# Kernel optimization log

Hardware: AMD Instinct MI355X
Metric: run time of the kernel (lower is better)

Reference implementation:

```python
import jax, jax.numpy as jnp
import numpy as np

B, S, D, H = 2, 2048, 1024, 16
HD = D // H

def setup_inputs() -> dict:
    key = jax.random.key(0)
    ks = jax.random.split(key, 9)
    s = 1.0 / np.sqrt(D)
    return {
        "x": jax.random.normal(ks[0], (B, S, D), jnp.float32),
        "Wq": jax.random.normal(ks[1], (D, D), jnp.float32) * s,
        "bq": jnp.zeros((D,), jnp.float32),
        "Wk": jax.random.normal(ks[2], (D, D), jnp.float32) * s,
        "bk": jnp.zeros((D,), jnp.float32),
        "Wv": jax.random.normal(ks[3], (D, D), jnp.float32) * s,
        "bv": jnp.zeros((D,), jnp.float32),
        "Wo": jax.random.normal(ks[4], (D, D), jnp.float32) * s,
        "bo": jnp.zeros((D,), jnp.float32),
    }

def reference(x, Wq, bq, Wk, bk, Wv, bv, Wo, bo):
    b, s, d = x.shape
    def split_heads(t):
        return t.reshape(b, s, H, HD).transpose(0, 2, 1, 3)  # [B,H,S,HD]
    q = split_heads(x @ Wq + bq)
    k = split_heads(x @ Wk + bk)
    v = split_heads(x @ Wv + bv)
    scores = jnp.einsum('bhqd,bhkd->bhqk', q, k) / jnp.sqrt(jnp.float32(HD))
    causal = jnp.tril(jnp.ones((s, s), bool))  # True = keep
    scores = jnp.where(causal, scores, -jnp.inf)
    attn = jax.nn.softmax(scores, axis=-1)
    out = jnp.einsum('bhqk,bhkd->bhqd', attn, v)  # [B,H,S,HD]
    out = out.transpose(0, 2, 1, 3).reshape(b, s, d)
    return out @ Wo + bo
```

## Files before the change

### kernel.cpp

```cpp
#include <hip/hip_runtime.h>

typedef unsigned short u16;
typedef unsigned int u32;
typedef __attribute__((ext_vector_type(8))) short bf16x8;
typedef __attribute__((ext_vector_type(4))) float f32x4;

#define BB 2
#define SS 2048
#define DD 1024
#define HH 16
#define HD 64
#define MM (BB * SS)

__device__ inline float u2f(u32 u) { return __uint_as_float(u); }
__device__ inline u16 f2bf(float f) {
  u32 u = __float_as_uint(f);
  return (u16)((u + 0x7fffu + ((u >> 16) & 1u)) >> 16);
}

__device__ inline int sw(int r, int ci) { return r * 64 + (((ci ^ (r & 7)) & 7) << 3); }

__global__ __launch_bounds__(256) void prep(const float* __restrict__ x, u16* __restrict__ xb,
                                            const float* __restrict__ W0, const float* __restrict__ W1,
                                            const float* __restrict__ W2, const float* __restrict__ W3,
                                            u16* __restrict__ Wt) {
  int z = blockIdx.z;
  int t = threadIdx.x;
  if (z >= 4) {
    int gid = (z - 4) * 256 + blockIdx.y * 16 + blockIdx.x;
    int i = (gid * 256 + t) * 8;
    float4 a = *(const float4*)(x + i);
    float4 b = *(const float4*)(x + i + 4);
    uint4 o;
    o.x = (u32)f2bf(a.x) | ((u32)f2bf(a.y) << 16);
    o.y = (u32)f2bf(a.z) | ((u32)f2bf(a.w) << 16);
    o.z = (u32)f2bf(b.x) | ((u32)f2bf(b.y) << 16);
    o.w = (u32)f2bf(b.z) | ((u32)f2bf(b.w) << 16);
    *(uint4*)(xb + i) = o;
    return;
  }
  const float* W = (z == 0) ? W0 : (z == 1) ? W1 : (z == 2) ? W2 : W3;
  u16* out = Wt + (size_t)z * (DD * DD);
  __shared__ __align__(16) u16 T[64][72];
  int n0 = blockIdx.x * 64, k0 = blockIdx.y * 64;
#pragma unroll
  for (int p = 0; p < 4; ++p) {
    int kr = (t >> 4) + p * 16;
    int c4 = (t & 15) * 4;
    float4 v = *(const float4*)&W[(size_t)(k0 + kr) * DD + n0 + c4];
    T[c4 + 0][kr] = f2bf(v.x);
    T[c4 + 1][kr] = f2bf(v.y);
    T[c4 + 2][kr] = f2bf(v.z);
    T[c4 + 3][kr] = f2bf(v.w);
  }
  __syncthreads();
#pragma unroll
  for (int p = 0; p < 2; ++p) {
    int n = (t >> 3) + p * 32;
    int c8 = (t & 7) * 8;
    uint4 v = *(const uint4*)&T[n][c8];
    *(uint4*)&out[(size_t)(n0 + n) * DD + k0 + c8] = v;
  }
}

__global__ __launch_bounds__(256, 3) void gemm_qkv(const u16* __restrict__ xb, const u16* __restrict__ Wt,
                                                   const float* __restrict__ bq, const float* __restrict__ bk,
                                                   const float* __restrict__ bv,
                                                   u16* __restrict__ Qb, u16* __restrict__ Kb, u16* __restrict__ Vtb) {
  __shared__ __align__(16) u16 As[2][128 * 32];
  __shared__ __align__(16) u16 Bs[2][128 * 32];
  const int tid = threadIdx.x, lane = tid & 63, wv = tid >> 6;
  const int wm = (wv >> 1) * 64, wn = (wv & 1) * 64;
  const int l16 = lane & 15, quad = lane >> 4;

  const int id = blockIdx.x;
  const int xcd = id & 7, inner = id >> 3;
  const int mg = xcd >> 1, ng = xcd & 1;
  const int im = inner & 7, rest = inner >> 3;
  const int in_ = rest & 3, z = rest >> 2;
  const int m0 = (mg * 8 + im) * 128, n0 = (ng * 4 + in_) * 128;

  const u16* Bt = Wt + (size_t)z * (DD * DD);
  const float* bias = (z == 0) ? bq : (z == 1) ? bk : bv;

  const int r0 = tid >> 2, k8 = (tid & 3) << 3;
  const u16* Ap0 = &xb[(size_t)(m0 + r0) * DD + k8];
  const u16* Ap1 = Ap0 + (size_t)64 * DD;
  const u16* Bp0 = &Bt[(size_t)(n0 + r0) * DD + k8];
  const u16* Bp1 = Bp0 + (size_t)64 * DD;

  uint4 a0 = *(const uint4*)Ap0, a1 = *(const uint4*)Ap1;
  uint4 b0 = *(const uint4*)Bp0, b1 = *(const uint4*)Bp1;
  *(uint4*)&As[0][r0 * 32 + k8] = a0;
  *(uint4*)&As[0][(r0 + 64) * 32 + k8] = a1;
  *(uint4*)&Bs[0][r0 * 32 + k8] = b0;
  *(uint4*)&Bs[0][(r0 + 64) * 32 + k8] = b1;
  a0 = *(const uint4*)(Ap0 + 32);
  a1 = *(const uint4*)(Ap1 + 32);
  b0 = *(const uint4*)(Bp0 + 32);
  b1 = *(const uint4*)(Bp1 + 32);
  __syncthreads();

  f32x4 acc[4][4];
  f32x4 zero = {0.f, 0.f, 0.f, 0.f};
#pragma unroll
  for (int i = 0; i < 4; ++i)
#pragma unroll
    for (int j = 0; j < 4; ++j) acc[i][j] = zero;

  for (int kk = 0; kk < 32; ++kk) {
    const int cur = (kk & 1) * 4096;
    bf16x8 af[4], bg[4];
#pragma unroll
    for (int i = 0; i < 4; ++i) {
      af[i] = *(const bf16x8*)&As[0][cur + (wm + i * 16 + l16) * 32 + quad * 8];
      bg[i] = *(const bf16x8*)&Bs[0][cur + (wn + i * 16 + l16) * 32 + quad * 8];
    }
#pragma unroll
    for (int i = 0; i < 4; ++i)
#pragma unroll
      for (int j = 0; j < 4; ++j)
        acc[i][j] = __builtin_amdgcn_mfma_f32_16x16x32_bf16(af[i], bg[j], acc[i][j], 0, 0, 0);
    if (kk + 1 < 32) {
      const int nxt = 4096 - cur;
      *(uint4*)&As[0][nxt + r0 * 32 + k8] = a0;
      *(uint4*)&As[0][nxt + (r0 + 64) * 32 + k8] = a1;
      *(uint4*)&Bs[0][nxt + r0 * 32 + k8] = b0;
      *(uint4*)&Bs[0][nxt + (r0 + 64) * 32 + k8] = b1;
      if (kk + 2 < 32) {
        int ko = (kk + 2) * 32;
        a0 = *(const uint4*)(Ap0 + ko);
        a1 = *(const uint4*)(Ap1 + ko);
        b0 = *(const uint4*)(Bp0 + ko);
        b1 = *(const uint4*)(Bp1 + ko);
      }
    }
    __syncthreads();
  }

  const float qsc = (z == 0) ? 0.180336880f : 1.0f;
  if (z == 2) {
#pragma unroll
    for (int i = 0; i < 4; ++i) {
#pragma unroll
      for (int j = 0; j < 4; ++j) {
        int col = n0 + wn + j * 16 + l16;
        float bcol = bias[col];
        int hh = col >> 6, dd = col & 63;
        int row0 = m0 + wm + i * 16 + quad * 4;
        int bb = row0 >> 11, s0 = row0 & (SS - 1);
        u32 w0 = (u32)f2bf(acc[i][j][0] + bcol) | ((u32)f2bf(acc[i][j][1] + bcol) << 16);
        u32 w1 = (u32)f2bf(acc[i][j][2] + bcol) | ((u32)f2bf(acc[i][j][3] + bcol) << 16);
        uint2 pk; pk.x = w0; pk.y = w1;
        *(uint2*)&Vtb[(((size_t)((bb * HH + hh) * HD + dd)) << 11) + s0] = pk;
      }
    }
  } else {
    u16* out = (z == 0) ? Qb : Kb;
#pragma unroll
    for (int i = 0; i < 4; ++i) {
#pragma unroll
      for (int j = 0; j < 4; ++j) {
        int col = n0 + wn + j * 16 + l16;
        float bcol = bias[col];
        int hh = col >> 6, dd = col & 63;
#pragma unroll
        for (int r = 0; r < 4; ++r) {
          int row = m0 + wm + i * 16 + quad * 4 + r;
          int bb = row >> 11, s = row & (SS - 1);
          out[((size_t)((bb * HH + hh) * SS + s) << 6) | dd] = f2bf((acc[i][j][r] + bcol) * qsc);
        }
      }
    }
  }
}

__global__ __launch_bounds__(256, 3) void gemm_out(const u16* __restrict__ Ub, const u16* __restrict__ Wot,
                                                   const float* __restrict__ bo, float* __restrict__ out) {
  __shared__ __align__(16) u16 As[2][128 * 32];
  __shared__ __align__(16) u16 Bs[2][64 * 32];
  const int tid = threadIdx.x, lane = tid & 63, wv = tid >> 6;
  const int wm = (wv >> 1) * 64, wn = (wv & 1) * 32;
  const int l16 = lane & 15, quad = lane >> 4;
  const int r0 = tid >> 2, k8 = (tid & 3) << 3;

  const int id = blockIdx.x;
  const int xcd = id & 7, inner = id >> 3;
  const int mg = xcd >> 1, ng = xcd & 1;
  const int im = inner & 7, in_ = inner >> 3;
  const int m0 = (mg * 8 + im) * 128, n0 = (ng * 8 + in_) * 64;

  const u16* Ap0 = &Ub[(size_t)(m0 + r0) * DD + k8];
  const u16* Ap1 = Ap0 + (size_t)64 * DD;
  const u16* Bp0 = &Wot[(size_t)(n0 + r0) * DD + k8];

  uint4 a0 = *(const uint4*)Ap0, a1 = *(const uint4*)Ap1, b0 = *(const uint4*)Bp0;
  *(uint4*)&As[0][r0 * 32 + k8] = a0;
  *(uint4*)&As[0][(r0 + 64) * 32 + k8] = a1;
  *(uint4*)&Bs[0][r0 * 32 + k8] = b0;
  a0 = *(const uint4*)(Ap0 + 32);
  a1 = *(const uint4*)(Ap1 + 32);
  b0 = *(const uint4*)(Bp0 + 32);
  __syncthreads();

  f32x4 acc[4][2];
  f32x4 zero = {0.f, 0.f, 0.f, 0.f};
#pragma unroll
  for (int i = 0; i < 4; ++i) { acc[i][0] = zero; acc[i][1] = zero; }

  for (int kk = 0; kk < 32; ++kk) {
    const int curA = (kk & 1) * 4096, curB = (kk & 1) * 2048;
    bf16x8 af[4], bg[2];
#pragma unroll
    for (int i = 0; i < 4; ++i) af[i] = *(const bf16x8*)&As[0][curA + (wm + i * 16 + l16) * 32 + quad * 8];
#pragma unroll
    for (int j = 0; j < 2; ++j) bg[j] = *(const bf16x8*)&Bs[0][curB + (wn + j * 16 + l16) * 32 + quad * 8];
#pragma unroll
    for (int i = 0; i < 4; ++i)
#pragma unroll
      for (int j = 0; j < 2; ++j)
        acc[i][j] = __builtin_amdgcn_mfma_f32_16x16x32_bf16(af[i], bg[j], acc[i][j], 0, 0, 0);
    if (kk + 1 < 32) {
      const int nxtA = 4096 - curA, nxtB = 2048 - curB;
      *(uint4*)&As[0][nxtA + r0 * 32 + k8] = a0;
      *(uint4*)&As[0][nxtA + (r0 + 64) * 32 + k8] = a1;
      *(uint4*)&Bs[0][nxtB + r0 * 32 + k8] = b0;
      if (kk + 2 < 32) {
        int ko = (kk + 2) * 32;
        a0 = *(const uint4*)(Ap0 + ko);
        a1 = *(const uint4*)(Ap1 + ko);
        b0 = *(const uint4*)(Bp0 + ko);
      }
    }
    __syncthreads();
  }

#pragma unroll
  for (int i = 0; i < 4; ++i) {
#pragma unroll
    for (int j = 0; j < 2; ++j) {
      int col = n0 + wn + j * 16 + l16;
      float bcol = bo[col];
#pragma unroll
      for (int r = 0; r < 4; ++r) {
        int row = m0 + wm + i * 16 + quad * 4 + r;
        out[(size_t)row * DD + col] = acc[i][j][r] + bcol;
      }
    }
  }
}

__global__ __launch_bounds__(256, 3) void attention_mfma(const u16* __restrict__ Q, const u16* __restrict__ K,
                                                         const u16* __restrict__ Vt, u16* __restrict__ Uo) {
  const int tid = threadIdx.x, lane = tid & 63, wv = tid >> 6;
  const int l16 = lane & 15, quad = lane >> 4;
  const int bh = blockIdx.x & 31;
  const int b = bh >> 4, h = bh & 15;
  const int qA = blockIdx.x >> 5;
  const int qB = 31 - qA;
  const int q0A = qA * 64, q0B = qB * 64;
  const u16* Qh = Q + (size_t)(b * HH + h) * SS * HD;
  const u16* Kh = K + (size_t)(b * HH + h) * SS * HD;
  const u16* Vh = Vt + (size_t)(b * HH + h) * HD * SS;

  __shared__ __align__(16) u16 K_lds[2][64 * 64];
  __shared__ __align__(16) u16 V_lds[2][64 * 64];
  __shared__ __align__(16) u16 p_lds[2][64][72];

  bf16x8 qfA0, qfA1, qfB0, qfB1;
  {
    const u16* qa = &Qh[(size_t)(q0A + wv * 16 + l16) * HD + quad * 8];
    qfA0 = *(const bf16x8*)qa;
    qfA1 = *(const bf16x8*)(qa + 32);
    const u16* qb = &Qh[(size_t)(q0B + wv * 16 + l16) * HD + quad * 8];
    qfB0 = *(const bf16x8*)qb;
    qfB1 = *(const bf16x8*)(qb + 32);
  }

  f32x4 zero = {0.f, 0.f, 0.f, 0.f};
  f32x4 oA[4], oB[4];
#pragma unroll
  for (int j = 0; j < 4; ++j) { oA[j] = zero; oB[j] = zero; }
  float lA[4] = {0.f, 0.f, 0.f, 0.f}, lB[4] = {0.f, 0.f, 0.f, 0.f};

  const int sr = tid >> 2, ci = tid & 3;
  const int cc = ci << 3;
  const u16* Kg = &Kh[(size_t)sr * HD + cc];
  const u16* Vg = &Vh[(size_t)sr * SS + cc];
  const int ktiles = qB + 1;
  const int wlo = sw(sr, ci), whi = sw(sr, ci + 4);

  uint4 ka = *(const uint4*)Kg, kb = *(const uint4*)(Kg + 32);
  uint4 va = *(const uint4*)Vg, vb = *(const uint4*)(Vg + 32);
  *(uint4*)&K_lds[0][wlo] = ka;
  *(uint4*)&K_lds[0][whi] = kb;
  *(uint4*)&V_lds[0][wlo] = va;
  *(uint4*)&V_lds[0][whi] = vb;
  {
    const u16* Kn = Kg + (size_t)64 * HD;
    const u16* Vn = Vg + 64;
    ka = *(const uint4*)Kn; kb = *(const uint4*)(Kn + 32);
    va = *(const uint4*)Vn; vb = *(const uint4*)(Vn + 32);
  }
  __syncthreads();

  for (int t = 0; t < ktiles; ++t) {
    const int cur = t & 1;
    const bool doA = (t <= qA);

    f32x4 sA[4], sB[4];
#pragma unroll
    for (int n = 0; n < 4; ++n) {
      const int kr = n * 16 + l16;
      bf16x8 kf0 = *(const bf16x8*)&K_lds[cur][sw(kr, quad)];
      bf16x8 kf1 = *(const bf16x8*)&K_lds[cur][sw(kr, quad + 4)];
      f32x4 aB = zero;
      aB = __builtin_amdgcn_mfma_f32_16x16x32_bf16(qfB0, kf0, aB, 0, 0, 0);
      aB = __builtin_amdgcn_mfma_f32_16x16x32_bf16(qfB1, kf1, aB, 0, 0, 0);
      sB[n] = aB;
      if (doA) {
        f32x4 aA = zero;
        aA = __builtin_amdgcn_mfma_f32_16x16x32_bf16(qfA0, kf0, aA, 0, 0, 0);
        aA = __builtin_amdgcn_mfma_f32_16x16x32_bf16(qfA1, kf1, aA, 0, 0, 0);
        sA[n] = aA;
      }
    }

    {
      const int rel = q0B + wv * 16 + quad * 4 - t * 64;
#pragma unroll
      for (int rr = 0; rr < 4; ++rr) {
        float p0 = __builtin_amdgcn_exp2f(sB[0][rr]);
        float p1 = __builtin_amdgcn_exp2f(sB[1][rr]);
        float p2 = __builtin_amdgcn_exp2f(sB[2][rr]);
        float p3 = __builtin_amdgcn_exp2f(sB[3][rr]);
        if (t == qB) {
          int row = rel + rr;
          p0 = (l16 <= row) ? p0 : 0.f;
          p1 = (16 + l16 <= row) ? p1 : 0.f;
          p2 = (32 + l16 <= row) ? p2 : 0.f;
          p3 = (48 + l16 <= row) ? p3 : 0.f;
        }
        lB[rr] += (p0 + p1) + (p2 + p3);
        u16* pr = p_lds[1][wv * 16 + quad * 4 + rr];
        pr[l16]      = (u16)(__float_as_uint(p0) >> 16);
        pr[16 + l16] = (u16)(__float_as_uint(p1) >> 16);
        pr[32 + l16] = (u16)(__float_as_uint(p2) >> 16);
        pr[48 + l16] = (u16)(__float_as_uint(p3) >> 16);
      }
    }
    if (doA) {
      const int rel = q0A + wv * 16 + quad * 4 - t * 64;
#pragma unroll
      for (int rr = 0; rr < 4; ++rr) {
        float p0 = __builtin_amdgcn_exp2f(sA[0][rr]);
        float p1 = __builtin_amdgcn_exp2f(sA[1][rr]);
        float p2 = __builtin_amdgcn_exp2f(sA[2][rr]);
        float p3 = __builtin_amdgcn_exp2f(sA[3][rr]);
        if (t == qA) {
          int row = rel + rr;
          p0 = (l16 <= row) ? p0 : 0.f;
          p1 = (16 + l16 <= row) ? p1 : 0.f;
          p2 = (32 + l16 <= row) ? p2 : 0.f;
          p3 = (48 + l16 <= row) ? p3 : 0.f;
        }
        lA[rr] += (p0 + p1) + (p2 + p3);
        u16* pr = p_lds[0][wv * 16 + quad * 4 + rr];
        pr[l16]      = (u16)(__float_as_uint(p0) >> 16);
        pr[16 + l16] = (u16)(__float_as_uint(p1) >> 16);
        pr[32 + l16] = (u16)(__float_as_uint(p2) >> 16);
        pr[48 + l16] = (u16)(__float_as_uint(p3) >> 16);
      }
    }

    if (doA) {
      bf16x8 pB0 = *(const bf16x8*)&p_lds[1][wv * 16 + l16][quad * 8];
      bf16x8 pB1 = *(const bf16x8*)&p_lds[1][wv * 16 + l16][32 + quad * 8];
      bf16x8 pA0 = *(const bf16x8*)&p_lds[0][wv * 16 + l16][quad * 8];
      bf16x8 pA1 = *(const bf16x8*)&p_lds[0][wv * 16 + l16][32 + quad * 8];
#pragma unroll
      for (int j = 0; j < 4; ++j) {
        const int vr = j * 16 + l16;
        bf16x8 vf0 = *(const bf16x8*)&V_lds[cur][sw(vr, quad)];
        bf16x8 vf1 = *(const bf16x8*)&V_lds[cur][sw(vr, quad + 4)];
        oB[j] = __builtin_amdgcn_mfma_f32_16x16x32_bf16(pB0, vf0, oB[j], 0, 0, 0);
        oB[j] = __builtin_amdgcn_mfma_f32_16x16x32_bf16(pB1, vf1, oB[j], 0, 0, 0);
        oA[j] = __builtin_amdgcn_mfma_f32_16x16x32_bf16(pA0, vf0, oA[j], 0, 0, 0);
        oA[j] = __builtin_amdgcn_mfma_f32_16x16x32_bf16(pA1, vf1, oA[j], 0, 0, 0);
      }
    } else {
      bf16x8 pB0 = *(const bf16x8*)&p_lds[1][wv * 16 + l16][quad * 8];
      bf16x8 pB1 = *(const bf16x8*)&p_lds[1][wv * 16 + l16][32 + quad * 8];
#pragma unroll
      for (int j = 0; j < 4; ++j) {
        const int vr = j * 16 + l16;
        bf16x8 vf0 = *(const bf16x8*)&V_lds[cur][sw(vr, quad)];
        bf16x8 vf1 = *(const bf16x8*)&V_lds[cur][sw(vr, quad + 4)];
        oB[j] = __builtin_amdgcn_mfma_f32_16x16x32_bf16(pB0, vf0, oB[j], 0, 0, 0);
        oB[j] = __builtin_amdgcn_mfma_f32_16x16x32_bf16(pB1, vf1, oB[j], 0, 0, 0);
      }
    }

    if (t + 1 < ktiles) {
      const int nxt = cur ^ 1;
      *(uint4*)&K_lds[nxt][wlo] = ka;
      *(uint4*)&K_lds[nxt][whi] = kb;
      *(uint4*)&V_lds[nxt][wlo] = va;
      *(uint4*)&V_lds[nxt][whi] = vb;
      if (t + 2 < ktiles) {
        const u16* Kn = Kg + (size_t)(t + 2) * 64 * HD;
        const u16* Vn = Vg + (t + 2) * 64;
        ka = *(const uint4*)Kn; kb = *(const uint4*)(Kn + 32);
        va = *(const uint4*)Vn; vb = *(const uint4*)(Vn + 32);
      }
    }
    __syncthreads();
  }

#pragma unroll
  for (int rr = 0; rr < 4; ++rr) {
    float a = lA[rr], c = lB[rr];
#pragma unroll
    for (int off = 1; off < 16; off <<= 1) {
      a += __shfl_xor(a, off);
      c += __shfl_xor(c, off);
    }
    lA[rr] = 1.0f / a;
    lB[rr] = 1.0f / c;
  }

#pragma unroll
  for (int j = 0; j < 4; ++j) {
#pragma unroll
    for (int r = 0; r < 4; ++r) {
      int rowA = q0A + wv * 16 + quad * 4 + r;
      int rowB = q0B + wv * 16 + quad * 4 + r;
      Uo[(size_t)(b * SS + rowA) * DD + (h << 6) + j * 16 + l16] = f2bf(oA[j][r] * lA[r]);
      Uo[(size_t)(b * SS + rowB) * DD + (h << 6) + j * 16 + l16] = f2bf(oB[j][r] * lB[r]);
    }
  }
}

extern "C" void kernel_launch(void* const* d_in, const int* in_sizes, int n_in,
                              void* d_out, int out_size, void* d_ws, size_t ws_size,
                              hipStream_t stream) {
  const float* x  = (const float*)d_in[0];
  const float* Wq = (const float*)d_in[1];
  const float* bq = (const float*)d_in[2];
  const float* Wk = (const float*)d_in[3];
  const float* bk = (const float*)d_in[4];
  const float* Wv = (const float*)d_in[5];
  const float* bv = (const float*)d_in[6];
  const float* Wo = (const float*)d_in[7];
  const float* bo = (const float*)d_in[8];
  float* out = (float*)d_out;

  char* ws = (char*)d_ws;
  u16* xb  = (u16*)(ws);
  u16* Wt  = (u16*)(ws + ((size_t)8 << 20));
  u16* Qb  = (u16*)(ws + ((size_t)16 << 20));
  u16* Kb  = (u16*)(ws + ((size_t)24 << 20));
  u16* Vtb = (u16*)(ws + ((size_t)32 << 20));
  u16* Ub  = (u16*)(ws + ((size_t)40 << 20));

  prep<<<dim3(16, 16, 12), dim3(256), 0, stream>>>(x, xb, Wq, Wk, Wv, Wo, Wt);
  gemm_qkv<<<dim3(768), dim3(256), 0, stream>>>(xb, Wt, bq, bk, bv, Qb, Kb, Vtb);
  attention_mfma<<<dim3(512), dim3(256), 0, stream>>>(Qb, Kb, Vtb, Ub);
  gemm_out<<<dim3(512), dim3(256), 0, stream>>>(Ub, Wt + (size_t)3 * DD * DD, bo, out);
}
```

Measured before the change: 195.9 us.

## Permute key order in P and V^T layouts to vectorize P stores to LDS

The softmax probabilities are packed into one 64-bit LDS store per row instead of four 16-bit stores, which puts keys in a permuted column order within P. To match, the V-transpose epilogue of the projection GEMM writes sequence positions in the same permuted order within each 64-key block, so the PV MFMA contraction stays consistent. This trades the V store (previously one packed 64-bit write) for four scattered 16-bit global writes. The attention kernel's occupancy hint is also lowered from 3 to 2 blocks per SM, giving the compiler more registers.

```diff
diff --git a/kernel.cpp b/kernel.cpp
--- a/kernel.cpp
+++ b/kernel.cpp
@@ -149,10 +149,11 @@
         int hh = col >> 6, dd = col & 63;
         int row0 = m0 + wm + i * 16 + quad * 4;
         int bb = row0 >> 11, s0 = row0 & (SS - 1);
-        u32 w0 = (u32)f2bf(acc[i][j][0] + bcol) | ((u32)f2bf(acc[i][j][1] + bcol) << 16);
-        u32 w1 = (u32)f2bf(acc[i][j][2] + bcol) | ((u32)f2bf(acc[i][j][3] + bcol) << 16);
-        uint2 pk; pk.x = w0; pk.y = w1;
-        *(uint2*)&Vtb[(((size_t)((bb * HH + hh) * HD + dd)) << 11) + s0] = pk;
+        int sbase = (s0 & ~63) + 16 * quad + ((s0 >> 4) & 3);
+        size_t base = (((size_t)((bb * HH + hh) * HD + dd)) << 11) + sbase;
+#pragma unroll
+        for (int r = 0; r < 4; ++r)
+          Vtb[base + 4 * r] = f2bf(acc[i][j][r] + bcol);
       }
     }
   } else {
@@ -250,7 +251,7 @@
   }
 }
 
-__global__ __launch_bounds__(256, 3) void attention_mfma(const u16* __restrict__ Q, const u16* __restrict__ K,
+__global__ __launch_bounds__(256, 2) void attention_mfma(const u16* __restrict__ Q, const u16* __restrict__ K,
                                                          const u16* __restrict__ Vt, u16* __restrict__ Uo) {
   const int tid = threadIdx.x, lane = tid & 63, wv = tid >> 6;
   const int l16 = lane & 15, quad = lane >> 4;
@@ -283,8 +284,7 @@
   for (int j = 0; j < 4; ++j) { oA[j] = zero; oB[j] = zero; }
   float lA[4] = {0.f, 0.f, 0.f, 0.f}, lB[4] = {0.f, 0.f, 0.f, 0.f};
 
-  const int sr = tid >> 2, ci = tid & 3;
-  const int cc = ci << 3;
+  const int sr = tid >> 2, ci = tid & 3, cc = ci << 3;
   const u16* Kg = &Kh[(size_t)sr * HD + cc];
   const u16* Vg = &Vh[(size_t)sr * SS + cc];
   const int ktiles = qB + 1;
@@ -342,11 +342,10 @@
           p3 = (48 + l16 <= row) ? p3 : 0.f;
         }
         lB[rr] += (p0 + p1) + (p2 + p3);
-        u16* pr = p_lds[1][wv * 16 + quad * 4 + rr];
-        pr[l16]      = (u16)(__float_as_uint(p0) >> 16);
-        pr[16 + l16] = (u16)(__float_as_uint(p1) >> 16);
-        pr[32 + l16] = (u16)(__float_as_uint(p2) >> 16);
-        pr[48 + l16] = (u16)(__float_as_uint(p3) >> 16);
+        uint2 pk;
+        pk.x = (__float_as_uint(p0) >> 16) | (__float_as_uint(p1) & 0xffff0000u);
+        pk.y = (__float_as_uint(p2) >> 16) | (__float_as_uint(p3) & 0xffff0000u);
+        *(uint2*)&p_lds[1][wv * 16 + quad * 4 + rr][l16 * 4] = pk;
       }
     }
     if (doA) {
@@ -365,11 +364,10 @@
           p3 = (48 + l16 <= row) ? p3 : 0.f;
         }
         lA[rr] += (p0 + p1) + (p2 + p3);
-        u16* pr = p_lds[0][wv * 16 + quad * 4 + rr];
-        pr[l16]      = (u16)(__float_as_uint(p0) >> 16);
-        pr[16 + l16] = (u16)(__float_as_uint(p1) >> 16);
-        pr[32 + l16] = (u16)(__float_as_uint(p2) >> 16);
-        pr[48 + l16] = (u16)(__float_as_uint(p3) >> 16);
+        uint2 pk;
+        pk.x = (__float_as_uint(p0) >> 16) | (__float_as_uint(p1) & 0xffff0000u);
+        pk.y = (__float_as_uint(p2) >> 16) | (__float_as_uint(p3) & 0xffff0000u);
+        *(uint2*)&p_lds[0][wv * 16 + quad * 4 + rr][l16 * 4] = pk;
       }
     }
 
```

Result: faster. 173.8 us (-11.3%).
